# Performance work log

Hardware: AMD Instinct MI355X
Metric: run time of the kernel (lower is better)

Reference implementation:

```python
import jax, jax.numpy as jnp
import numpy as np

TAU = 2.0
V_TH = 1.0


def setup_inputs() -> dict:
    key = jax.random.key(0)
    k_x, k_w1, k_w2 = jax.random.split(key, 3)
    T, B, N = 128, 64, 1024
    x = jax.random.normal(k_x, (T, B, N), dtype=jnp.float32)
    # nn.Linear(hidden, hidden, bias=False) weights: [out, in]
    scale = 1.0 / np.sqrt(N)
    w1 = jax.random.uniform(k_w1, (N, N), dtype=jnp.float32, minval=-scale, maxval=scale)
    w2 = jax.random.uniform(k_w2, (N, N), dtype=jnp.float32, minval=-scale, maxval=scale)
    return {"x": x, "w1": w1, "w2": w2}


def reference(x, w1, w2):
    # x: [T, B, N]; Linear with weight [out, in] -> x @ W^T
    T, B, N = x.shape
    h = jnp.einsum('tbn,mn->tbm', x, w1)  # fc1 applied per timestep

    def lif_step(v, h_t):
        # v: [B, N] membrane state; h_t: [B, N] input current
        hv = v + (h_t - v) / TAU
        s = (hv >= V_TH).astype(h_t.dtype)  # hard threshold spike
        v_next = hv * (1.0 - s)             # reset-to-zero on spike
        return v_next, s

    v0 = jnp.zeros((B, N), dtype=x.dtype)
    _, spikes = jax.lax.scan(lif_step, v0, h)  # spikes: [T, B, N]

    return jnp.einsum('tbn,mn->tbm', spikes, w2)  # fc2
```

## Files before the change

### kernel.cpp

```cpp
#include <hip/hip_runtime.h>
#include <hip/hip_bf16.h>

#define TT 128
#define BB 64
#define NN 1024

typedef __attribute__((ext_vector_type(4))) float f32x4;
typedef __attribute__((ext_vector_type(8))) short bf16x8;

#define FLAG_THR 2e-4
#define MAX_FLAG 16384

__device__ __forceinline__ unsigned short bf_hi_rne(float f, float& rem) {
    union { float f; unsigned int u; } c; c.f = f;
    const unsigned int r = c.u + 0x7fffu + ((c.u >> 16) & 1u);
    const unsigned short h = (unsigned short)(r >> 16);
    union { unsigned int u; float f; } b; b.u = ((unsigned int)h) << 16;
    rem = f - b.f;
    return h;
}

__global__ __launch_bounds__(256) void split_k(const float* __restrict__ X,
                                               unsigned short* __restrict__ XHi,
                                               unsigned short* __restrict__ XLo,
                                               const float* __restrict__ W,
                                               unsigned short* __restrict__ WHi,
                                               unsigned short* __restrict__ WLo,
                                               const float* __restrict__ W2,
                                               float* __restrict__ W2T,
                                               int* __restrict__ cnt) {
    __shared__ float tile[32][33];
    if (blockIdx.x == 0 && threadIdx.x == 0) *cnt = 0;

    if (blockIdx.x >= 9216) {
        const int tblk = blockIdx.x - 9216;
        const int tx  = threadIdx.x & 31;
        const int ty4 = (threadIdx.x >> 5) * 4;
        const int c0 = (tblk & 31) * 32;
        const int r0 = (tblk >> 5) * 32;
#pragma unroll
        for (int i = 0; i < 4; ++i)
            tile[ty4 + i][tx] = W2[(size_t)(r0 + ty4 + i) * NN + c0 + tx];
        __syncthreads();
#pragma unroll
        for (int i = 0; i < 4; ++i)
            W2T[(size_t)(c0 + ty4 + i) * NN + r0 + tx] = tile[tx][ty4 + i];
        return;
    }

    const bool isX = blockIdx.x < 8192;
    const float* A = isX ? X : W;
    unsigned short* Hi = isX ? XHi : WHi;
    unsigned short* Lo = isX ? XLo : WLo;
    const size_t blk = isX ? blockIdx.x : (blockIdx.x - 8192);
    const size_t f = (blk * 256 + threadIdx.x) * 4;
    const float4 v = *(const float4*)(A + f);
    float r, r2;
    ushort4 hi, lo;
    hi.x = bf_hi_rne(v.x, r); lo.x = bf_hi_rne(r, r2);
    hi.y = bf_hi_rne(v.y, r); lo.y = bf_hi_rne(r, r2);
    hi.z = bf_hi_rne(v.z, r); lo.z = bf_hi_rne(r, r2);
    hi.w = bf_hi_rne(v.w, r); lo.w = bf_hi_rne(r, r2);
    *(ushort4*)(Hi + f) = hi;
    *(ushort4*)(Lo + f) = lo;
}

__global__ __launch_bounds__(512, 4) void gemm1_lif(
    const unsigned short* __restrict__ A0g, const unsigned short* __restrict__ A1g,
    const unsigned short* __restrict__ B0g, const unsigned short* __restrict__ B1g,
    unsigned long long* __restrict__ M, int* __restrict__ counter,
    int* __restrict__ list) {
    __shared__ unsigned short ldsbuf[2][4][128 * 32];

    const int tid  = threadIdx.x;
    const int wave = tid >> 6;
    const int lane = tid & 63;

    const int bid = blockIdx.x;
    const int pos = bid >> 3;
    const int bm  = (bid & 7) * 8 + (pos >> 3);
    const int bn  = pos & 7;

    const int wm = (wave >> 2) * 64;
    const int wn = (wave & 3) * 32;

    f32x4 acc[4][2];
#pragma unroll
    for (int i = 0; i < 4; ++i)
#pragma unroll
        for (int j = 0; j < 2; ++j) acc[i][j] = (f32x4){0.f, 0.f, 0.f, 0.f};

    const int buf = wave >> 1;
    const unsigned short* gsrc =
        (buf == 0) ? A0g : (buf == 1) ? A1g : (buf == 2) ? B0g : B1g;
    const bool isA = (buf < 2);
    const int shalf = (wave & 1) * 256;

#define STAGE(BI, KT)                                                         \
    {                                                                         \
        _Pragma("unroll")                                                     \
        for (int q = 0; q < 4; ++q) {                                         \
            const int slot = shalf + q * 64 + lane;                           \
            const int row  = slot >> 2;                                       \
            const int kc   = (slot & 3) ^ ((row >> 1) & 3);                   \
            const size_t grow = isA ? ((size_t)row * 64 + bm)                 \
                                    : ((size_t)bn * 128 + row);               \
            const unsigned short* gp =                                        \
                gsrc + grow * NN + (KT) * 32 + kc * 8;                        \
            __builtin_amdgcn_global_load_lds(                                 \
                (const __attribute__((address_space(1))) void*)gp,            \
                (__attribute__((address_space(3))) void*)(                    \
                    &ldsbuf[BI][buf][(wave & 1) * 2048 + q * 512]),           \
                16, 0, 0);                                                    \
        }                                                                     \
    }

#define COMPUTE(BI)                                                           \
    {                                                                         \
        const int c  = lane >> 4;                                             \
        const int rA = lane & 15;                                             \
        bf16x8 a0[4], a1[4], b0[2], b1[2];                                    \
        _Pragma("unroll")                                                     \
        for (int mf = 0; mf < 4; ++mf) {                                      \
            const int row = wm + mf * 16 + rA;                                \
            const int kc  = c ^ ((row >> 1) & 3);                             \
            a0[mf] = *(const bf16x8*)(&ldsbuf[BI][0][row * 32 + kc * 8]);     \
            a1[mf] = *(const bf16x8*)(&ldsbuf[BI][1][row * 32 + kc * 8]);     \
        }                                                                     \
        _Pragma("unroll")                                                     \
        for (int nf = 0; nf < 2; ++nf) {                                      \
            const int row = wn + nf * 16 + rA;                                \
            const int kc  = c ^ ((row >> 1) & 3);                             \
            b0[nf] = *(const bf16x8*)(&ldsbuf[BI][2][row * 32 + kc * 8]);     \
            b1[nf] = *(const bf16x8*)(&ldsbuf[BI][3][row * 32 + kc * 8]);     \
        }                                                                     \
        _Pragma("unroll")                                                     \
        for (int mf = 0; mf < 4; ++mf)                                        \
            _Pragma("unroll")                                                 \
            for (int nf = 0; nf < 2; ++nf) {                                  \
                acc[mf][nf] = __builtin_amdgcn_mfma_f32_16x16x32_bf16(        \
                    a0[mf], b0[nf], acc[mf][nf], 0, 0, 0);                    \
                acc[mf][nf] = __builtin_amdgcn_mfma_f32_16x16x32_bf16(        \
                    a0[mf], b1[nf], acc[mf][nf], 0, 0, 0);                    \
                acc[mf][nf] = __builtin_amdgcn_mfma_f32_16x16x32_bf16(        \
                    a1[mf], b0[nf], acc[mf][nf], 0, 0, 0);                    \
            }                                                                 \
    }

#define WAIT4 asm volatile("s_waitcnt vmcnt(4)" ::: "memory")
#define WAIT0 asm volatile("s_waitcnt vmcnt(0)" ::: "memory")
#define BAR   __builtin_amdgcn_s_barrier()
#define SCHED0 __builtin_amdgcn_sched_barrier(0)

    STAGE(0, 0);
    STAGE(1, 1);

    for (int kt = 0; kt < 30; kt += 2) {
        WAIT4; BAR; SCHED0;
        COMPUTE(0);
        BAR;
        STAGE(0, kt + 2);
        WAIT4; BAR; SCHED0;
        COMPUTE(1);
        BAR;
        STAGE(1, kt + 3);
    }
    WAIT4; BAR; SCHED0;
    COMPUTE(0);
    BAR;
    WAIT0; BAR; SCHED0;
    COMPUTE(1);

#undef STAGE
#undef COMPUTE
#undef WAIT4
#undef WAIT0
#undef BAR
#undef SCHED0

    __syncthreads();
    float* htile = (float*)&ldsbuf[0][0][0];

    const int cr = lane >> 4, cc = lane & 15;
#pragma unroll
    for (int mf = 0; mf < 4; ++mf)
#pragma unroll
        for (int nf = 0; nf < 2; ++nf)
#pragma unroll
            for (int r = 0; r < 4; ++r) {
                const int t   = wm + mf * 16 + cr * 4 + r;
                const int col = wn + nf * 16 + cc;
                htile[t * 128 + col] = acc[mf][nf][r];
            }
    __syncthreads();

    if (tid < 128) {
        const int col = tid;
        const int wv  = tid >> 6;
        double v = 0.0;
        bool flagged = false;
#pragma unroll 8
        for (int t = 0; t < TT; ++t) {
            const float hcur = htile[t * 128 + col];
            const double hv = v + ((double)hcur - v) * 0.5;
            const bool s = (hv >= 1.0);
            flagged = flagged || (fabs(hv - 1.0) < FLAG_THR);
            const unsigned long long bmask = __ballot(s);
            if (lane == 0)
                M[(size_t)t * 1024 + bm * 16 + bn * 2 + wv] = bmask;
            v = s ? 0.0 : hv;
        }
        if (flagged) {
            const int idx = atomicAdd(counter, 1);
            if (idx < MAX_FLAG) list[idx] = bm * 1024 + bn * 128 + col;
        }
    }
}

#define KT 32
#define SA 132
#define SB 68
__global__ __launch_bounds__(256) void gemm1_f64(const float* __restrict__ X,
                                                 const float* __restrict__ W1,
                                                 float* __restrict__ H) {
    __shared__ float As[KT][SA];
    __shared__ float Bs[KT][SB];
    const int tid = threadIdx.x;
    const int bm  = blockIdx.y;
    const int bn  = blockIdx.x;
    const int tm  = tid >> 4;
    const int tn  = tid & 15;
    const int lrow = tid >> 3;
    const int lk4  = (tid & 7) << 2;
    double acc[8][4];
#pragma unroll
    for (int i = 0; i < 8; ++i)
#pragma unroll
        for (int j = 0; j < 4; ++j) acc[i][j] = 0.0;
    for (int kt = 0; kt < NN; kt += KT) {
#pragma unroll
        for (int p = 0; p < 4; ++p) {
            const int m = lrow + p * 32;
            const float4 v = *(const float4*)&X[(size_t)(bm * 128 + m) * NN + kt + lk4];
            As[lk4 + 0][m] = v.x; As[lk4 + 1][m] = v.y;
            As[lk4 + 2][m] = v.z; As[lk4 + 3][m] = v.w;
        }
#pragma unroll
        for (int p = 0; p < 2; ++p) {
            const int n = lrow + p * 32;
            const float4 v = *(const float4*)&W1[(size_t)(bn * 64 + n) * NN + kt + lk4];
            Bs[lk4 + 0][n] = v.x; Bs[lk4 + 1][n] = v.y;
            Bs[lk4 + 2][n] = v.z; Bs[lk4 + 3][n] = v.w;
        }
        __syncthreads();
#pragma unroll
        for (int k = 0; k < KT; ++k) {
            float a[8], b[4];
            *(float4*)&a[0] = *(const float4*)&As[k][tm * 8];
            *(float4*)&a[4] = *(const float4*)&As[k][tm * 8 + 4];
            *(float4*)&b[0] = *(const float4*)&Bs[k][tn * 4];
#pragma unroll
            for (int i = 0; i < 8; ++i)
#pragma unroll
                for (int j = 0; j < 4; ++j)
                    acc[i][j] = fma((double)a[i], (double)b[j], acc[i][j]);
        }
        __syncthreads();
    }
#pragma unroll
    for (int i = 0; i < 8; ++i) {
        float4 v;
        v.x = (float)acc[i][0]; v.y = (float)acc[i][1];
        v.z = (float)acc[i][2]; v.w = (float)acc[i][3];
        *(float4*)&H[(size_t)(bm * 128 + tm * 8 + i) * NN + bn * 64 + tn * 4] = v;
    }
}

__global__ __launch_bounds__(256) void transp_k(const float* __restrict__ A,
                                                float* __restrict__ B) {
    __shared__ float tile[32][33];
    const int tx  = threadIdx.x & 31;
    const int ty4 = (threadIdx.x >> 5) * 4;
    const int c0 = blockIdx.x * 32;
    const int r0 = blockIdx.y * 32;
#pragma unroll
    for (int i = 0; i < 4; ++i)
        tile[ty4 + i][tx] = A[(size_t)(r0 + ty4 + i) * NN + c0 + tx];
    __syncthreads();
#pragma unroll
    for (int i = 0; i < 4; ++i)
        B[(size_t)(c0 + ty4 + i) * NN + r0 + tx] = tile[tx][ty4 + i];
}

__global__ __launch_bounds__(256) void lif_k(const float* __restrict__ H,
                                             unsigned long long* __restrict__ M,
                                             int* __restrict__ counter,
                                             int* __restrict__ list) {
    const int e    = blockIdx.x * 256 + threadIdx.x;
    const int lane = threadIdx.x & 63;
    const int word = e >> 6;
    double v = 0.0;
    bool flagged = false;

    float buf[8];
#pragma unroll
    for (int i = 0; i < 8; ++i) buf[i] = H[(size_t)i * 65536 + e];

#pragma unroll 8
    for (int t = 0; t < TT; ++t) {
        const float hcur = buf[t & 7];
        if (t + 8 < TT) buf[t & 7] = H[(size_t)(t + 8) * 65536 + e];
        const double hv = v + ((double)hcur - v) * 0.5;
        const bool s = (hv >= 1.0);
        flagged = flagged || (fabs(hv - 1.0) < FLAG_THR);
        const unsigned long long bmask = __ballot(s);
        if (lane == 0) M[(size_t)t * 1024 + word] = bmask;
        v = s ? 0.0 : hv;
    }
    if (flagged) {
        const int idx = atomicAdd(counter, 1);
        if (idx < MAX_FLAG) list[idx] = e;
    }
}

__global__ __launch_bounds__(256) void fixup_dots_k(const float* __restrict__ X,
                                                    const float* __restrict__ W1,
                                                    const int* __restrict__ counter,
                                                    const int* __restrict__ list,
                                                    double* __restrict__ sbuf) {
    const int nw   = (gridDim.x * 256) >> 6;
    const int wid  = (blockIdx.x * 256 + threadIdx.x) >> 6;
    const int lane = threadIdx.x & 63;
    int cnt = *counter; if (cnt > MAX_FLAG) cnt = MAX_FLAG;
    const int total = cnt * 16;

    for (int item = wid; item < total; item += nw) {
        const int ci = item >> 4;
        const int tc = item & 15;
        const int e = list[ci];
        const int b = e >> 10, n = e & 1023;
        double wk[16];
        {
            const float4* wr = (const float4*)(W1 + (size_t)n * NN);
#pragma unroll
            for (int j = 0; j < 4; ++j) {
                const float4 wv = wr[lane + 64 * j];
                wk[4 * j + 0] = (double)wv.x; wk[4 * j + 1] = (double)wv.y;
                wk[4 * j + 2] = (double)wv.z; wk[4 * j + 3] = (double)wv.w;
            }
        }
#pragma unroll
        for (int tt = 0; tt < 8; ++tt) {
            const int t = tc * 8 + tt;
            const float4* xr = (const float4*)(X + (size_t)(t * 64 + b) * NN);
            double s = 0.0;
#pragma unroll
            for (int j = 0; j < 4; ++j) {
                const float4 xv = xr[lane + 64 * j];
                s = fma((double)xv.x, wk[4 * j + 0], s);
                s = fma((double)xv.y, wk[4 * j + 1], s);
                s = fma((double)xv.z, wk[4 * j + 2], s);
                s = fma((double)xv.w, wk[4 * j + 3], s);
            }
#pragma unroll
            for (int off = 32; off > 0; off >>= 1) s += __shfl_xor(s, off);
            if (lane == 0) sbuf[(size_t)ci * 128 + t] = s;
        }
    }
}

__global__ __launch_bounds__(64) void fixup_scan_k(const double* __restrict__ sbuf,
                                                   const int* __restrict__ counter,
                                                   const int* __restrict__ list,
                                                   unsigned long long* __restrict__ M) {
    __shared__ double sv[128];
    __shared__ unsigned char sp[128];
    const int lane = threadIdx.x;
    int cnt = *counter; if (cnt > MAX_FLAG) cnt = MAX_FLAG;

    for (int ci = blockIdx.x; ci < cnt; ci += gridDim.x) {
        const int e = list[ci];
        sv[lane]      = sbuf[(size_t)ci * 128 + lane];
        sv[lane + 64] = sbuf[(size_t)ci * 128 + 64 + lane];
        __syncthreads();
        if (lane == 0) {
            double v = 0.0;
#pragma unroll
            for (int t = 0; t < TT; ++t) {
                const double hv = v + (sv[t] - v) * 0.5;
                const bool s = (hv >= 1.0);
                sp[t] = s;
                v = s ? 0.0 : hv;
            }
        }
        __syncthreads();
        const unsigned long long bit = 1ull << (e & 63);
        const size_t wbase = (size_t)(e >> 6);
#pragma unroll
        for (int p = 0; p < 2; ++p) {
            const int t = lane + p * 64;
            unsigned long long* mp = &M[(size_t)t * 1024 + wbase];
            if (sp[t]) atomicOr(mp, bit);
            else       atomicAnd(mp, ~bit);
        }
        __syncthreads();
    }
}

__global__ __launch_bounds__(256) void spmm2_k(const unsigned long long* __restrict__ M,
                                               const float* __restrict__ W2T,
                                               float* __restrict__ OUT) {
    __shared__ unsigned long long sm[16];
    const int r   = blockIdx.x;
    const int tid = threadIdx.x;
    if (tid < 16) sm[tid] = M[(size_t)r * 16 + tid];
    __syncthreads();

    double a0 = 0.0, a1 = 0.0, a2 = 0.0, a3 = 0.0;
    for (int w = 0; w < 16; ++w) {
        unsigned long long bits = sm[w];
        while (bits) {
            const int l = __builtin_ctzll(bits);
            bits &= bits - 1;
            const int n = w * 64 + l;
            const float4 wv = *(const float4*)&W2T[(size_t)n * NN + tid * 4];
            a0 += (double)wv.x; a1 += (double)wv.y;
            a2 += (double)wv.z; a3 += (double)wv.w;
        }
    }
    float4 o;
    o.x = (float)a0; o.y = (float)a1; o.z = (float)a2; o.w = (float)a3;
    *(float4*)&OUT[(size_t)r * NN + tid * 4] = o;
}

extern "C" void kernel_launch(void* const* d_in, const int* in_sizes, int n_in,
                              void* d_out, int out_size, void* d_ws, size_t ws_size,
                              hipStream_t stream) {
    const float* x  = (const float*)d_in[0];
    const float* w1 = (const float*)d_in[1];
    const float* w2 = (const float*)d_in[2];
    float* out = (float*)d_out;
    char* ws = (char*)d_ws;

    const size_t oH = 0, oW2T = 33554432, oM = 37748736;
    const size_t oB0 = 38797312, oB1 = 40894464;
    const size_t oA0 = 42991616, oA1 = 59768832;
    const size_t oCnt = 76546048, oList = 76546304;
    const size_t needFull = 76808448;

    float* h   = (float*)(ws + oH);
    float* w2t = (float*)(ws + oW2T);
    unsigned long long* masks = (unsigned long long*)(ws + oM);

    if (ws_size >= needFull) {
        unsigned short* B0s = (unsigned short*)(ws + oB0);
        unsigned short* B1s = (unsigned short*)(ws + oB1);
        unsigned short* A0g = (unsigned short*)(ws + oA0);
        unsigned short* A1g = (unsigned short*)(ws + oA1);
        int* cnt  = (int*)(ws + oCnt);
        int* list = (int*)(ws + oList);
        double* sbuf = (double*)(ws + oA0);

        split_k<<<10240, 256, 0, stream>>>(x, A0g, A1g, w1, B0s, B1s, w2, w2t, cnt);
        gemm1_lif<<<512, 512, 0, stream>>>(A0g, A1g, B0s, B1s, masks, cnt, list);
        fixup_dots_k<<<256, 256, 0, stream>>>(x, w1, cnt, list, sbuf);
        fixup_scan_k<<<256, 64, 0, stream>>>(sbuf, cnt, list, masks);
        spmm2_k<<<8192, 256, 0, stream>>>(masks, w2t, out);
    } else {
        int* cnt  = (int*)(ws + 38797312);
        int* list = (int*)(ws + 38797568);
        gemm1_f64<<<dim3(16, 64), 256, 0, stream>>>(x, w1, h);
        transp_k<<<dim3(32, 32), 256, 0, stream>>>(w2, w2t);
        hipMemsetAsync(cnt, 0, 4, stream);
        lif_k<<<256, 256, 0, stream>>>(h, masks, cnt, list);
        spmm2_k<<<8192, 256, 0, stream>>>(masks, w2t, out);
    }
}
```

Measured before the change: 99.37 us.

## Fuse X bf16 hi/lo split into GEMM1 A-tile loading

The separate pre-pass that split X into bf16 high and low halves in global memory is removed. GEMM1 now loads fp32 X directly into registers, splits it, and writes both halves into LDS, while B still goes through direct global-to-LDS loads. This avoids writing and rereading about 32 MB of split X, but adds conversion work and register pressure inside the GEMM pipeline and changes its wait scheme. The h-tile LDS writes and reads are also XOR-swizzled to reduce bank conflicts in the LIF scan.

```diff
diff --git a/kernel.cpp b/kernel.cpp
--- a/kernel.cpp
+++ b/kernel.cpp
@@ -20,10 +20,25 @@
     return h;
 }
 
-__global__ __launch_bounds__(256) void split_k(const float* __restrict__ X,
-                                               unsigned short* __restrict__ XHi,
-                                               unsigned short* __restrict__ XLo,
-                                               const float* __restrict__ W,
+__device__ __forceinline__ unsigned int pack_hi2(float a, float b,
+                                                 float& la, float& lb) {
+    union { float f; unsigned int u; } ca, cb;
+    ca.f = a; cb.f = b;
+    const unsigned int ha = (ca.u + 0x7fffu + ((ca.u >> 16) & 1u)) >> 16;
+    const unsigned int hb = (cb.u + 0x7fffu + ((cb.u >> 16) & 1u)) >> 16;
+    union { unsigned int u; float f; } fa, fb;
+    fa.u = ha << 16; fb.u = hb << 16;
+    la = a - fa.f; lb = b - fb.f;
+    return ha | (hb << 16);
+}
+__device__ __forceinline__ unsigned int pack_bf2(float a, float b) {
+    union { float f; unsigned int u; } ca, cb;
+    ca.f = a; cb.f = b;
+    return ((ca.u + 0x7fffu + ((ca.u >> 16) & 1u)) >> 16) |
+           (((cb.u + 0x7fffu + ((cb.u >> 16) & 1u)) >> 16) << 16);
+}
+
+__global__ __launch_bounds__(256) void split_k(const float* __restrict__ W,
                                                unsigned short* __restrict__ WHi,
                                                unsigned short* __restrict__ WLo,
                                                const float* __restrict__ W2,
@@ -32,8 +47,8 @@
     __shared__ float tile[32][33];
     if (blockIdx.x == 0 && threadIdx.x == 0) *cnt = 0;
 
-    if (blockIdx.x >= 9216) {
-        const int tblk = blockIdx.x - 9216;
+    if (blockIdx.x >= 1024) {
+        const int tblk = blockIdx.x - 1024;
         const int tx  = threadIdx.x & 31;
         const int ty4 = (threadIdx.x >> 5) * 4;
         const int c0 = (tblk & 31) * 32;
@@ -48,25 +63,20 @@
         return;
     }
 
-    const bool isX = blockIdx.x < 8192;
-    const float* A = isX ? X : W;
-    unsigned short* Hi = isX ? XHi : WHi;
-    unsigned short* Lo = isX ? XLo : WLo;
-    const size_t blk = isX ? blockIdx.x : (blockIdx.x - 8192);
-    const size_t f = (blk * 256 + threadIdx.x) * 4;
-    const float4 v = *(const float4*)(A + f);
+    const size_t f = ((size_t)blockIdx.x * 256 + threadIdx.x) * 4;
+    const float4 v = *(const float4*)(W + f);
     float r, r2;
     ushort4 hi, lo;
     hi.x = bf_hi_rne(v.x, r); lo.x = bf_hi_rne(r, r2);
     hi.y = bf_hi_rne(v.y, r); lo.y = bf_hi_rne(r, r2);
     hi.z = bf_hi_rne(v.z, r); lo.z = bf_hi_rne(r, r2);
     hi.w = bf_hi_rne(v.w, r); lo.w = bf_hi_rne(r, r2);
-    *(ushort4*)(Hi + f) = hi;
-    *(ushort4*)(Lo + f) = lo;
+    *(ushort4*)(WHi + f) = hi;
+    *(ushort4*)(WLo + f) = lo;
 }
 
 __global__ __launch_bounds__(512, 4) void gemm1_lif(
-    const unsigned short* __restrict__ A0g, const unsigned short* __restrict__ A1g,
+    const float* __restrict__ X,
     const unsigned short* __restrict__ B0g, const unsigned short* __restrict__ B1g,
     unsigned long long* __restrict__ M, int* __restrict__ counter,
     int* __restrict__ list) {
@@ -90,27 +100,48 @@
 #pragma unroll
         for (int j = 0; j < 2; ++j) acc[i][j] = (f32x4){0.f, 0.f, 0.f, 0.f};
 
-    const int buf = wave >> 1;
-    const unsigned short* gsrc =
-        (buf == 0) ? A0g : (buf == 1) ? A1g : (buf == 2) ? B0g : B1g;
-    const bool isA = (buf < 2);
-    const int shalf = (wave & 1) * 256;
-
-#define STAGE(BI, KT)                                                         \
+    const int arow = tid >> 2;
+    const int ac   = tid & 3;
+    const int apc  = ac ^ ((arow >> 1) & 3);
+    const float* xs = X + (size_t)(arow * 64 + bm) * NN + ac * 8;
+    const int aoff = arow * 32 + apc * 8;
+
+    const int bbuf = 2 + (wave >> 2);
+    const unsigned short* bsrc = (wave < 4) ? B0g : B1g;
+    const int bq0 = (wave & 3) * 128;
+
+#define AISSUE(R0, R1, KT)                                                    \
+    {                                                                         \
+        R0 = *(const float4*)(xs + (KT) * 32);                                \
+        R1 = *(const float4*)(xs + (KT) * 32 + 4);                            \
+    }
+
+#define AWRITE(BI, R0, R1)                                                    \
+    {                                                                         \
+        float l0, l1, l2, l3, l4, l5, l6, l7;                                 \
+        const unsigned int h0 = pack_hi2(R0.x, R0.y, l0, l1);                 \
+        const unsigned int h1 = pack_hi2(R0.z, R0.w, l2, l3);                 \
+        const unsigned int h2 = pack_hi2(R1.x, R1.y, l4, l5);                 \
+        const unsigned int h3 = pack_hi2(R1.z, R1.w, l6, l7);                 \
+        const unsigned int q0 = pack_bf2(l0, l1), q1 = pack_bf2(l2, l3);      \
+        const unsigned int q2 = pack_bf2(l4, l5), q3 = pack_bf2(l6, l7);      \
+        *(uint4*)(&ldsbuf[BI][0][aoff]) = make_uint4(h0, h1, h2, h3);         \
+        *(uint4*)(&ldsbuf[BI][1][aoff]) = make_uint4(q0, q1, q2, q3);         \
+    }
+
+#define BSTAGE(BI, KT)                                                        \
     {                                                                         \
         _Pragma("unroll")                                                     \
-        for (int q = 0; q < 4; ++q) {                                         \
-            const int slot = shalf + q * 64 + lane;                           \
+        for (int q = 0; q < 2; ++q) {                                         \
+            const int slot = bq0 + q * 64 + lane;                             \
             const int row  = slot >> 2;                                       \
             const int kc   = (slot & 3) ^ ((row >> 1) & 3);                   \
-            const size_t grow = isA ? ((size_t)row * 64 + bm)                 \
-                                    : ((size_t)bn * 128 + row);               \
             const unsigned short* gp =                                        \
-                gsrc + grow * NN + (KT) * 32 + kc * 8;                        \
+                bsrc + (size_t)(bn * 128 + row) * NN + (KT) * 32 + kc * 8;    \
             __builtin_amdgcn_global_load_lds(                                 \
                 (const __attribute__((address_space(1))) void*)gp,            \
                 (__attribute__((address_space(3))) void*)(                    \
-                    &ldsbuf[BI][buf][(wave & 1) * 2048 + q * 512]),           \
+                    &ldsbuf[BI][bbuf][(bq0 + q * 64) * 8]),                   \
                 16, 0, 0);                                                    \
         }                                                                     \
     }
@@ -147,34 +178,47 @@
             }                                                                 \
     }
 
-#define WAIT4 asm volatile("s_waitcnt vmcnt(4)" ::: "memory")
-#define WAIT0 asm volatile("s_waitcnt vmcnt(0)" ::: "memory")
+#define LGKM0 asm volatile("s_waitcnt lgkmcnt(0)" ::: "memory")
+#define VM0   asm volatile("s_waitcnt vmcnt(0)" ::: "memory")
 #define BAR   __builtin_amdgcn_s_barrier()
 #define SCHED0 __builtin_amdgcn_sched_barrier(0)
 
-    STAGE(0, 0);
-    STAGE(1, 1);
+    float4 ae0, ae1, ao0, ao1;
+
+    AISSUE(ae0, ae1, 0);
+    BSTAGE(0, 0);
+    AISSUE(ao0, ao1, 1);
+    BSTAGE(1, 1);
+    AWRITE(0, ae0, ae1);
 
     for (int kt = 0; kt < 30; kt += 2) {
-        WAIT4; BAR; SCHED0;
+        AWRITE(1, ao0, ao1);
+        AISSUE(ae0, ae1, kt + 2);
+        LGKM0; BAR; SCHED0;
         COMPUTE(0);
         BAR;
-        STAGE(0, kt + 2);
-        WAIT4; BAR; SCHED0;
+        BSTAGE(0, kt + 2);
+        AWRITE(0, ae0, ae1);
+        AISSUE(ao0, ao1, kt + 3);
+        LGKM0; BAR; SCHED0;
         COMPUTE(1);
         BAR;
-        STAGE(1, kt + 3);
-    }
-    WAIT4; BAR; SCHED0;
+        BSTAGE(1, kt + 3);
+    }
+    AWRITE(1, ao0, ao1);
+    LGKM0; BAR; SCHED0;
     COMPUTE(0);
     BAR;
-    WAIT0; BAR; SCHED0;
+    VM0;
+    LGKM0; BAR; SCHED0;
     COMPUTE(1);
 
-#undef STAGE
+#undef AISSUE
+#undef AWRITE
+#undef BSTAGE
 #undef COMPUTE
-#undef WAIT4
-#undef WAIT0
+#undef LGKM0
+#undef VM0
 #undef BAR
 #undef SCHED0
 
@@ -190,7 +234,7 @@
             for (int r = 0; r < 4; ++r) {
                 const int t   = wm + mf * 16 + cr * 4 + r;
                 const int col = wn + nf * 16 + cc;
-                htile[t * 128 + col] = acc[mf][nf][r];
+                htile[t * 128 + (col ^ ((t & 7) << 2))] = acc[mf][nf][r];
             }
     __syncthreads();
 
@@ -201,7 +245,7 @@
         bool flagged = false;
 #pragma unroll 8
         for (int t = 0; t < TT; ++t) {
-            const float hcur = htile[t * 128 + col];
+            const float hcur = htile[t * 128 + (col ^ ((t & 7) << 2))];
             const double hv = v + ((double)hcur - v) * 0.5;
             const bool s = (hv >= 1.0);
             flagged = flagged || (fabs(hv - 1.0) < FLAG_THR);
@@ -444,7 +488,7 @@
 
     const size_t oH = 0, oW2T = 33554432, oM = 37748736;
     const size_t oB0 = 38797312, oB1 = 40894464;
-    const size_t oA0 = 42991616, oA1 = 59768832;
+    const size_t oA0 = 42991616;
     const size_t oCnt = 76546048, oList = 76546304;
     const size_t needFull = 76808448;
 
@@ -455,14 +499,12 @@
     if (ws_size >= needFull) {
         unsigned short* B0s = (unsigned short*)(ws + oB0);
         unsigned short* B1s = (unsigned short*)(ws + oB1);
-        unsigned short* A0g = (unsigned short*)(ws + oA0);
-        unsigned short* A1g = (unsigned short*)(ws + oA1);
         int* cnt  = (int*)(ws + oCnt);
         int* list = (int*)(ws + oList);
         double* sbuf = (double*)(ws + oA0);
 
-        split_k<<<10240, 256, 0, stream>>>(x, A0g, A1g, w1, B0s, B1s, w2, w2t, cnt);
-        gemm1_lif<<<512, 512, 0, stream>>>(A0g, A1g, B0s, B1s, masks, cnt, list);
+        split_k<<<2048, 256, 0, stream>>>(w1, B0s, B1s, w2, w2t, cnt);
+        gemm1_lif<<<512, 512, 0, stream>>>(x, B0s, B1s, masks, cnt, list);
         fixup_dots_k<<<256, 256, 0, stream>>>(x, w1, cnt, list, sbuf);
         fixup_scan_k<<<256, 64, 0, stream>>>(sbuf, cnt, list, masks);
         spmm2_k<<<8192, 256, 0, stream>>>(masks, w2t, out);
```

Result: no change. 100.9 us (+1.5%).

## Fuse fixup dot and scan kernels and swizzle LIF h-tile LDS layout

Applied to the files above, without the earlier changes.

The two fixup kernels (f64 dot products into a scratch buffer, then a separate scan) become one kernel, fixup_m_k. It computes each flagged neuron's 128 timestep dots in one 512-thread block, runs the LIF scan and patches the spike masks in place. This removes a kernel launch and the scratch round trip, but runs on only 64 blocks, so parallelism over flagged items is lower. The h-tile stored in LDS after the GEMM also gets an XOR column swizzle keyed on the timestep, meant to cut bank conflicts in the accumulator writes.

```diff
diff --git a/kernel.cpp b/kernel.cpp
--- a/kernel.cpp
+++ b/kernel.cpp
@@ -64,37 +64,6 @@
     *(ushort4*)(Hi + f) = hi;
     *(ushort4*)(Lo + f) = lo;
 }
-
-__global__ __launch_bounds__(512, 4) void gemm1_lif(
-    const unsigned short* __restrict__ A0g, const unsigned short* __restrict__ A1g,
-    const unsigned short* __restrict__ B0g, const unsigned short* __restrict__ B1g,
-    unsigned long long* __restrict__ M, int* __restrict__ counter,
-    int* __restrict__ list) {
-    __shared__ unsigned short ldsbuf[2][4][128 * 32];
-
-    const int tid  = threadIdx.x;
-    const int wave = tid >> 6;
-    const int lane = tid & 63;
-
-    const int bid = blockIdx.x;
-    const int pos = bid >> 3;
-    const int bm  = (bid & 7) * 8 + (pos >> 3);
-    const int bn  = pos & 7;
-
-    const int wm = (wave >> 2) * 64;
-    const int wn = (wave & 3) * 32;
-
-    f32x4 acc[4][2];
-#pragma unroll
-    for (int i = 0; i < 4; ++i)
-#pragma unroll
-        for (int j = 0; j < 2; ++j) acc[i][j] = (f32x4){0.f, 0.f, 0.f, 0.f};
-
-    const int buf = wave >> 1;
-    const unsigned short* gsrc =
-        (buf == 0) ? A0g : (buf == 1) ? A1g : (buf == 2) ? B0g : B1g;
-    const bool isA = (buf < 2);
-    const int shalf = (wave & 1) * 256;
 
 #define STAGE(BI, KT)                                                         \
     {                                                                         \
@@ -149,34 +118,56 @@
 
 #define WAIT4 asm volatile("s_waitcnt vmcnt(4)" ::: "memory")
 #define WAIT0 asm volatile("s_waitcnt vmcnt(0)" ::: "memory")
-#define BAR   __builtin_amdgcn_s_barrier()
+#define BARX   __builtin_amdgcn_s_barrier()
 #define SCHED0 __builtin_amdgcn_sched_barrier(0)
+
+__global__ __launch_bounds__(512, 4) void gemm1_lif_k(
+    const unsigned short* __restrict__ A0g, const unsigned short* __restrict__ A1g,
+    const unsigned short* __restrict__ B0g, const unsigned short* __restrict__ B1g,
+    unsigned long long* __restrict__ M, int* __restrict__ counter,
+    int* __restrict__ list) {
+    __shared__ unsigned short ldsbuf[2][4][128 * 32];
+
+    const int tid  = threadIdx.x;
+    const int wave = tid >> 6;
+    const int lane = tid & 63;
+    const int bid = blockIdx.x;
+    const int pos = bid >> 3;
+    const int bm  = (bid & 7) * 8 + (pos >> 3);
+    const int bn  = pos & 7;
+    const int wm = (wave >> 2) * 64;
+    const int wn = (wave & 3) * 32;
+
+    f32x4 acc[4][2];
+#pragma unroll
+    for (int i = 0; i < 4; ++i)
+#pragma unroll
+        for (int j = 0; j < 2; ++j) acc[i][j] = (f32x4){0.f, 0.f, 0.f, 0.f};
+
+    const int buf = wave >> 1;
+    const unsigned short* gsrc =
+        (buf == 0) ? A0g : (buf == 1) ? A1g : (buf == 2) ? B0g : B1g;
+    const bool isA = (buf < 2);
+    const int shalf = (wave & 1) * 256;
 
     STAGE(0, 0);
     STAGE(1, 1);
 
     for (int kt = 0; kt < 30; kt += 2) {
-        WAIT4; BAR; SCHED0;
+        WAIT4; BARX; SCHED0;
         COMPUTE(0);
-        BAR;
+        BARX;
         STAGE(0, kt + 2);
-        WAIT4; BAR; SCHED0;
+        WAIT4; BARX; SCHED0;
         COMPUTE(1);
-        BAR;
+        BARX;
         STAGE(1, kt + 3);
     }
-    WAIT4; BAR; SCHED0;
+    WAIT4; BARX; SCHED0;
     COMPUTE(0);
-    BAR;
-    WAIT0; BAR; SCHED0;
+    BARX;
+    WAIT0; BARX; SCHED0;
     COMPUTE(1);
-
-#undef STAGE
-#undef COMPUTE
-#undef WAIT4
-#undef WAIT0
-#undef BAR
-#undef SCHED0
 
     __syncthreads();
     float* htile = (float*)&ldsbuf[0][0][0];
@@ -190,7 +181,7 @@
             for (int r = 0; r < 4; ++r) {
                 const int t   = wm + mf * 16 + cr * 4 + r;
                 const int col = wn + nf * 16 + cc;
-                htile[t * 128 + col] = acc[mf][nf][r];
+                htile[t * 128 + (col ^ ((t & 7) << 2))] = acc[mf][nf][r];
             }
     __syncthreads();
 
@@ -201,7 +192,7 @@
         bool flagged = false;
 #pragma unroll 8
         for (int t = 0; t < TT; ++t) {
-            const float hcur = htile[t * 128 + col];
+            const float hcur = htile[t * 128 + (col ^ ((t & 7) << 2))];
             const double hv = v + ((double)hcur - v) * 0.5;
             const bool s = (hv >= 1.0);
             flagged = flagged || (fabs(hv - 1.0) < FLAG_THR);
@@ -215,6 +206,82 @@
             if (idx < MAX_FLAG) list[idx] = bm * 1024 + bn * 128 + col;
         }
     }
+}
+
+__global__ __launch_bounds__(512) void fixup_m_k(
+    const float* __restrict__ X, const float* __restrict__ W1,
+    unsigned long long* __restrict__ M, const int* __restrict__ counter,
+    const int* __restrict__ list) {
+    __shared__ double sv[128];
+    __shared__ unsigned char sp[128];
+    const int tid_ = threadIdx.x;
+    int cnt_ = *counter; if (cnt_ > MAX_FLAG) cnt_ = MAX_FLAG;
+
+    for (int ci = blockIdx.x; ci < cnt_; ci += gridDim.x) {
+        const int e = list[ci];
+        const int b = e >> 10, n = e & 1023;
+        const int t_ = tid_ >> 2, q_ = tid_ & 3;
+        const float4* xr = (const float4*)(X + (size_t)(t_ * 64 + b) * NN) + q_ * 64;
+        const float4* wr = (const float4*)(W1 + (size_t)n * NN) + q_ * 64;
+        double s = 0.0;
+#pragma unroll 8
+        for (int j = 0; j < 64; ++j) {
+            const float4 xv = xr[j];
+            const float4 wv = wr[j];
+            s = fma((double)xv.x, (double)wv.x, s);
+            s = fma((double)xv.y, (double)wv.y, s);
+            s = fma((double)xv.z, (double)wv.z, s);
+            s = fma((double)xv.w, (double)wv.w, s);
+        }
+        s += __shfl_xor(s, 1);
+        s += __shfl_xor(s, 2);
+        if (q_ == 0) sv[t_] = s;
+        __syncthreads();
+        if (tid_ == 0) {
+            double v = 0.0;
+#pragma unroll
+            for (int t = 0; t < TT; ++t) {
+                const double hv = v + (sv[t] - v) * 0.5;
+                const bool sf = (hv >= 1.0);
+                sp[t] = sf;
+                v = sf ? 0.0 : hv;
+            }
+        }
+        __syncthreads();
+        if (tid_ < 128) {
+            const unsigned long long bit = 1ull << (e & 63);
+            unsigned long long* mp = &M[(size_t)tid_ * 1024 + (e >> 6)];
+            if (sp[tid_]) atomicOr(mp, bit);
+            else          atomicAnd(mp, ~bit);
+        }
+        __syncthreads();
+    }
+}
+
+__global__ __launch_bounds__(256) void spmm2_k(const unsigned long long* __restrict__ M,
+                                               const float* __restrict__ W2T,
+                                               float* __restrict__ OUT) {
+    __shared__ unsigned long long sm[16];
+    const int r   = blockIdx.x;
+    const int tid = threadIdx.x;
+    if (tid < 16) sm[tid] = M[(size_t)r * 16 + tid];
+    __syncthreads();
+
+    double a0 = 0.0, a1 = 0.0, a2 = 0.0, a3 = 0.0;
+    for (int w = 0; w < 16; ++w) {
+        unsigned long long bits = sm[w];
+        while (bits) {
+            const int l = __builtin_ctzll(bits);
+            bits &= bits - 1;
+            const int n = w * 64 + l;
+            const float4 wv = *(const float4*)&W2T[(size_t)n * NN + tid * 4];
+            a0 += (double)wv.x; a1 += (double)wv.y;
+            a2 += (double)wv.z; a3 += (double)wv.w;
+        }
+    }
+    float4 o;
+    o.x = (float)a0; o.y = (float)a1; o.z = (float)a2; o.w = (float)a3;
+    *(float4*)&OUT[(size_t)r * NN + tid * 4] = o;
 }
 
 #define KT 32
@@ -323,116 +390,6 @@
     }
 }
 
-__global__ __launch_bounds__(256) void fixup_dots_k(const float* __restrict__ X,
-                                                    const float* __restrict__ W1,
-                                                    const int* __restrict__ counter,
-                                                    const int* __restrict__ list,
-                                                    double* __restrict__ sbuf) {
-    const int nw   = (gridDim.x * 256) >> 6;
-    const int wid  = (blockIdx.x * 256 + threadIdx.x) >> 6;
-    const int lane = threadIdx.x & 63;
-    int cnt = *counter; if (cnt > MAX_FLAG) cnt = MAX_FLAG;
-    const int total = cnt * 16;
-
-    for (int item = wid; item < total; item += nw) {
-        const int ci = item >> 4;
-        const int tc = item & 15;
-        const int e = list[ci];
-        const int b = e >> 10, n = e & 1023;
-        double wk[16];
-        {
-            const float4* wr = (const float4*)(W1 + (size_t)n * NN);
-#pragma unroll
-            for (int j = 0; j < 4; ++j) {
-                const float4 wv = wr[lane + 64 * j];
-                wk[4 * j + 0] = (double)wv.x; wk[4 * j + 1] = (double)wv.y;
-                wk[4 * j + 2] = (double)wv.z; wk[4 * j + 3] = (double)wv.w;
-            }
-        }
-#pragma unroll
-        for (int tt = 0; tt < 8; ++tt) {
-            const int t = tc * 8 + tt;
-            const float4* xr = (const float4*)(X + (size_t)(t * 64 + b) * NN);
-            double s = 0.0;
-#pragma unroll
-            for (int j = 0; j < 4; ++j) {
-                const float4 xv = xr[lane + 64 * j];
-                s = fma((double)xv.x, wk[4 * j + 0], s);
-                s = fma((double)xv.y, wk[4 * j + 1], s);
-                s = fma((double)xv.z, wk[4 * j + 2], s);
-                s = fma((double)xv.w, wk[4 * j + 3], s);
-            }
-#pragma unroll
-            for (int off = 32; off > 0; off >>= 1) s += __shfl_xor(s, off);
-            if (lane == 0) sbuf[(size_t)ci * 128 + t] = s;
-        }
-    }
-}
-
-__global__ __launch_bounds__(64) void fixup_scan_k(const double* __restrict__ sbuf,
-                                                   const int* __restrict__ counter,
-                                                   const int* __restrict__ list,
-                                                   unsigned long long* __restrict__ M) {
-    __shared__ double sv[128];
-    __shared__ unsigned char sp[128];
-    const int lane = threadIdx.x;
-    int cnt = *counter; if (cnt > MAX_FLAG) cnt = MAX_FLAG;
-
-    for (int ci = blockIdx.x; ci < cnt; ci += gridDim.x) {
-        const int e = list[ci];
-        sv[lane]      = sbuf[(size_t)ci * 128 + lane];
-        sv[lane + 64] = sbuf[(size_t)ci * 128 + 64 + lane];
-        __syncthreads();
-        if (lane == 0) {
-            double v = 0.0;
-#pragma unroll
-            for (int t = 0; t < TT; ++t) {
-                const double hv = v + (sv[t] - v) * 0.5;
-                const bool s = (hv >= 1.0);
-                sp[t] = s;
-                v = s ? 0.0 : hv;
-            }
-        }
-        __syncthreads();
-        const unsigned long long bit = 1ull << (e & 63);
-        const size_t wbase = (size_t)(e >> 6);
-#pragma unroll
-        for (int p = 0; p < 2; ++p) {
-            const int t = lane + p * 64;
-            unsigned long long* mp = &M[(size_t)t * 1024 + wbase];
-            if (sp[t]) atomicOr(mp, bit);
-            else       atomicAnd(mp, ~bit);
-        }
-        __syncthreads();
-    }
-}
-
-__global__ __launch_bounds__(256) void spmm2_k(const unsigned long long* __restrict__ M,
-                                               const float* __restrict__ W2T,
-                                               float* __restrict__ OUT) {
-    __shared__ unsigned long long sm[16];
-    const int r   = blockIdx.x;
-    const int tid = threadIdx.x;
-    if (tid < 16) sm[tid] = M[(size_t)r * 16 + tid];
-    __syncthreads();
-
-    double a0 = 0.0, a1 = 0.0, a2 = 0.0, a3 = 0.0;
-    for (int w = 0; w < 16; ++w) {
-        unsigned long long bits = sm[w];
-        while (bits) {
-            const int l = __builtin_ctzll(bits);
-            bits &= bits - 1;
-            const int n = w * 64 + l;
-            const float4 wv = *(const float4*)&W2T[(size_t)n * NN + tid * 4];
-            a0 += (double)wv.x; a1 += (double)wv.y;
-            a2 += (double)wv.z; a3 += (double)wv.w;
-        }
-    }
-    float4 o;
-    o.x = (float)a0; o.y = (float)a1; o.z = (float)a2; o.w = (float)a3;
-    *(float4*)&OUT[(size_t)r * NN + tid * 4] = o;
-}
-
 extern "C" void kernel_launch(void* const* d_in, const int* in_sizes, int n_in,
                               void* d_out, int out_size, void* d_ws, size_t ws_size,
                               hipStream_t stream) {
@@ -459,12 +416,10 @@
         unsigned short* A1g = (unsigned short*)(ws + oA1);
         int* cnt  = (int*)(ws + oCnt);
         int* list = (int*)(ws + oList);
-        double* sbuf = (double*)(ws + oA0);
 
         split_k<<<10240, 256, 0, stream>>>(x, A0g, A1g, w1, B0s, B1s, w2, w2t, cnt);
-        gemm1_lif<<<512, 512, 0, stream>>>(A0g, A1g, B0s, B1s, masks, cnt, list);
-        fixup_dots_k<<<256, 256, 0, stream>>>(x, w1, cnt, list, sbuf);
-        fixup_scan_k<<<256, 64, 0, stream>>>(sbuf, cnt, list, masks);
+        gemm1_lif_k<<<512, 512, 0, stream>>>(A0g, A1g, B0s, B1s, masks, cnt, list);
+        fixup_m_k<<<64, 512, 0, stream>>>(x, w1, masks, cnt, list);
         spmm2_k<<<8192, 256, 0, stream>>>(masks, w2t, out);
     } else {
         int* cnt  = (int*)(ws + 38797312);
```

After: 121.8 us. 22.5% more time.
